# Kernel optimization log

Measured on AMD Instinct MI355X. Metric: run time of the kernel, lower is better.

## Reference

```python
import jax, jax.numpy as jnp
import numpy as np

STRIDE = 1
PADDING = 1


def sign_ste(w):
    # forward: 2*(w>0)-1 ; backward: identity (straight-through estimator)
    s = 2.0 * (w > 0.0).astype(w.dtype) - 1.0
    return w + jax.lax.stop_gradient(s - w)


def setup_inputs() -> dict:
    key = jax.random.key(0)
    kx, kw = jax.random.split(key)
    x = jax.random.normal(kx, (32, 256, 56, 56), dtype=jnp.float32)
    # mirror torch.rand(shape) * 0.001
    weight = jax.random.uniform(kw, (256, 256, 3, 3), dtype=jnp.float32) * 0.001
    return {"x": x, "weight": weight}


def reference(x, weight):
    # per-output-channel scaling factor: mean |w| over (in, kh, kw), detached
    scaling = jnp.mean(jnp.abs(weight), axis=(1, 2, 3), keepdims=True)  # [O,1,1,1]
    scaling = jax.lax.stop_gradient(scaling)
    binary_weights = scaling * sign_ste(weight)
    y = jax.lax.conv_general_dilated(
        x, binary_weights,
        window_strides=(STRIDE, STRIDE),
        padding=[(PADDING, PADDING), (PADDING, PADDING)],
        dimension_numbers=("NCHW", "OIHW", "NCHW"),
    )
    return y
```

## Files before the change

kernel.cpp:

```cpp
#include <hip/hip_runtime.h>
#include <stdint.h>


typedef float f32x4 __attribute__((ext_vector_type(4)));

__global__ __launch_bounds__(256) void stage1(const float* __restrict__ x,
                                              f32x4* __restrict__ u16,
                                              const float* __restrict__ w,
                                              float* __restrict__ scale,
                                              int* __restrict__ nneg,
                                              int* __restrict__ negidx) {
    __shared__ float red[4];
    __shared__ int cnt;
    if (blockIdx.x < 1568) {
        const int id  = blockIdx.x * 256 + threadIdx.x;
        const int n   = id / 12544;
        const int rem = id - n * 12544;
        const int g   = rem / 784;
        const int hw4 = rem - g * 784;
        const f32x4* xp =
            (const f32x4*)(x + (size_t)(n * 256 + g * 16) * 3136) + hw4;
        f32x4 s = {0.f, 0.f, 0.f, 0.f};
#pragma unroll
        for (int c = 0; c < 16; ++c)
            s += __builtin_nontemporal_load(xp + c * 784);
        u16[id] = s;
    } else {
        const int o = blockIdx.x - 1568, i = threadIdx.x;
        if (i == 0) cnt = 0;
        __syncthreads();
        const float* wp = w + ((size_t)o * 256 + i) * 9;
        float s = 0.f;
#pragma unroll
        for (int k = 0; k < 9; ++k) {
            const float v = wp[k];
            s += fabsf(v);
            if (v <= 0.f) {
                const int slot = atomicAdd(&cnt, 1);
                negidx[o * 2304 + slot] = i * 9 + k;
            }
        }
#pragma unroll
        for (int off = 32; off > 0; off >>= 1) s += __shfl_down(s, off);
        if ((i & 63) == 0) red[i >> 6] = s;
        __syncthreads();
        if (i == 0) {
            scale[o] = (red[0] + red[1] + red[2] + red[3]) * (1.0f / 2304.0f);
            nneg[o]  = cnt;
        }
    }
}

__global__ __launch_bounds__(256) void boxsum(const float* __restrict__ u16,
                                              float* __restrict__ T) {
    __shared__ float Us[336];
    const int n  = blockIdx.x / 14;
    const int h0 = (blockIdx.x - n * 14) * 4;
    const float* base = u16 + (size_t)n * 16 * 3136;
    for (int idx = threadIdx.x; idx < 336; idx += 256) {
        const int lr = idx / 56, col = idx - lr * 56;
        const int h = h0 - 1 + lr;
        float s = 0.f;
        if (h >= 0 && h < 56) {
            const float* bp = base + h * 56 + col;
#pragma unroll
            for (int g = 0; g < 16; ++g) s += bp[g * 3136];
        }
        Us[idx] = s;
    }
    __syncthreads();
    float* Tn = T + (size_t)n * 3136;
    for (int idx = threadIdx.x; idx < 224; idx += 256) {
        const int lr = idx / 56, w = idx - lr * 56;
        float acc = 0.f;
#pragma unroll
        for (int r = 0; r < 3; ++r) {
            const float* row = Us + (lr + r) * 56;
            if (w > 0)  acc += row[w - 1];
            acc += row[w];
            if (w < 55) acc += row[w + 1];
        }
        Tn[(h0 + lr) * 56 + w] = acc;
    }
}

__global__ __launch_bounds__(256) void yout(const float* __restrict__ T,
                                            const float* __restrict__ scale,
                                            const int* __restrict__ nneg,
                                            const int* __restrict__ negidx,
                                            const float* __restrict__ x,
                                            float* __restrict__ out) {
    const int b = blockIdx.x;
    const int o = b & 255, n = b >> 8;
    const float sc = scale[o];
    const f32x4* Tn = (const f32x4*)(T + (size_t)n * 3136);
    f32x4* op = (f32x4*)(out + ((size_t)n * 256 + o) * 3136);
    if (nneg[o] == 0) {
#pragma unroll
        for (int j = 0; j < 4; ++j) {
            const int hw4 = threadIdx.x + j * 256;
            if (hw4 >= 784) break;
            f32x4 v = Tn[hw4] * sc;
            __builtin_nontemporal_store(v, op + hw4);
        }
    } else {
        const int nn = nneg[o];
        const float c2 = 2.f * sc;
#pragma unroll
        for (int j = 0; j < 4; ++j) {
            const int hw4 = threadIdx.x + j * 256;
            if (hw4 >= 784) break;
            f32x4 v = Tn[hw4] * sc;
            for (int q = 0; q < nn; ++q) {
                const int iof = negidx[o * 2304 + q];
                const int i = iof / 9, rs = iof - i * 9;
                const int r = rs / 3 - 1, s2 = rs - (rs / 3) * 3 - 1;
                const float* xpl = x + ((size_t)n * 256 + i) * 3136;
#pragma unroll
                for (int e = 0; e < 4; ++e) {
                    const int hw = hw4 * 4 + e;
                    const int h = hw / 56 + r, ww = hw - (hw / 56) * 56 + s2;
                    const float xv = (h >= 0 && h < 56 && ww >= 0 && ww < 56)
                                         ? xpl[h * 56 + ww] : 0.f;
                    v[e] -= c2 * xv;
                }
            }
            __builtin_nontemporal_store(v, op + hw4);
        }
    }
}

extern "C" void kernel_launch(void* const* d_in, const int* in_sizes, int n_in,
                              void* d_out, int out_size, void* d_ws, size_t ws_size,
                              hipStream_t stream) {
    const float* x = (const float*)d_in[0];
    const float* w = (const float*)d_in[1];
    float* out = (float*)d_out;

    char* ws = (char*)d_ws;
    size_t off = 0;
    float* u16 = (float*)(ws + off);
    off += (size_t)32 * 16 * 3136 * 4;
    float* T = (float*)(ws + off);
    off += (size_t)32 * 3136 * 4;
    float* scale = (float*)(ws + off);
    off += 256 * 4;
    int* nneg = (int*)(ws + off);
    off += 256 * 4;
    int* negidx = (int*)(ws + off);

    stage1<<<dim3(1824), 256, 0, stream>>>(x, (f32x4*)u16, w, scale, nneg, negidx);
    boxsum<<<dim3(448), 256, 0, stream>>>(u16, T);
    yout<<<dim3(8192), 256, 0, stream>>>(T, scale, nneg, negidx, x, out);
}
```

Baseline: 178.3 us.

## Fuse box-sum and output-broadcast kernels into one per-row-tile kernel

Merges the boxsum and yout kernels into a single kernel. Each of the 448 blocks computes a 4-row tile of the 3x3 box sum into shared memory, then loops over all 256 output channels, writing scale*T plus any negative-weight corrections. This removes the global T buffer round trip and one kernel launch. In exchange the writes become scalar per-thread stores issued from far fewer blocks, each running a 256-iteration serial loop, which may reduce memory-level parallelism for the large output write.

```diff
diff --git a/kernel.cpp b/kernel.cpp
--- a/kernel.cpp
+++ b/kernel.cpp
@@ -51,13 +51,25 @@
     }
 }
 
-__global__ __launch_bounds__(256) void boxsum(const float* __restrict__ u16,
-                                              float* __restrict__ T) {
+__global__ __launch_bounds__(256) void boxout(const float* __restrict__ u16,
+                                              const float* __restrict__ scale,
+                                              const int* __restrict__ nneg,
+                                              const int* __restrict__ negidx,
+                                              const float* __restrict__ x,
+                                              float* __restrict__ out) {
     __shared__ float Us[336];
+    __shared__ float Tls[224];
+    __shared__ float ssc[256];
+    __shared__ int   snn[256];
     const int n  = blockIdx.x / 14;
     const int h0 = (blockIdx.x - n * 14) * 4;
+    const int t  = threadIdx.x;
+
+    ssc[t] = scale[t];
+    snn[t] = nneg[t];
+
     const float* base = u16 + (size_t)n * 16 * 3136;
-    for (int idx = threadIdx.x; idx < 336; idx += 256) {
+    for (int idx = t; idx < 336; idx += 256) {
         const int lr = idx / 56, col = idx - lr * 56;
         const int h = h0 - 1 + lr;
         float s = 0.f;
@@ -69,9 +81,8 @@
         Us[idx] = s;
     }
     __syncthreads();
-    float* Tn = T + (size_t)n * 3136;
-    for (int idx = threadIdx.x; idx < 224; idx += 256) {
-        const int lr = idx / 56, w = idx - lr * 56;
+    if (t < 224) {
+        const int lr = t / 56, w = t - lr * 56;
         float acc = 0.f;
 #pragma unroll
         for (int r = 0; r < 3; ++r) {
@@ -80,53 +91,32 @@
             acc += row[w];
             if (w < 55) acc += row[w + 1];
         }
-        Tn[(h0 + lr) * 56 + w] = acc;
+        Tls[t] = acc;
     }
-}
+    __syncthreads();
 
-__global__ __launch_bounds__(256) void yout(const float* __restrict__ T,
-                                            const float* __restrict__ scale,
-                                            const int* __restrict__ nneg,
-                                            const int* __restrict__ negidx,
-                                            const float* __restrict__ x,
-                                            float* __restrict__ out) {
-    const int b = blockIdx.x;
-    const int o = b & 255, n = b >> 8;
-    const float sc = scale[o];
-    const f32x4* Tn = (const f32x4*)(T + (size_t)n * 3136);
-    f32x4* op = (f32x4*)(out + ((size_t)n * 256 + o) * 3136);
-    if (nneg[o] == 0) {
-#pragma unroll
-        for (int j = 0; j < 4; ++j) {
-            const int hw4 = threadIdx.x + j * 256;
-            if (hw4 >= 784) break;
-            f32x4 v = Tn[hw4] * sc;
-            __builtin_nontemporal_store(v, op + hw4);
-        }
-    } else {
-        const int nn = nneg[o];
-        const float c2 = 2.f * sc;
-#pragma unroll
-        for (int j = 0; j < 4; ++j) {
-            const int hw4 = threadIdx.x + j * 256;
-            if (hw4 >= 784) break;
-            f32x4 v = Tn[hw4] * sc;
+    const float tv = (t < 224) ? Tls[t] : 0.f;
+    const int lr = t / 56, w = t - lr * 56, h = h0 + lr;
+    float* obase = out + (size_t)n * 256 * 3136 + h0 * 56;
+    for (int o = 0; o < 256; ++o) {
+        const float sc = ssc[o];
+        float v = sc * tv;
+        const int nn = snn[o];
+        if (nn > 0) {
+            const float c2 = 2.f * sc;
             for (int q = 0; q < nn; ++q) {
                 const int iof = negidx[o * 2304 + q];
                 const int i = iof / 9, rs = iof - i * 9;
                 const int r = rs / 3 - 1, s2 = rs - (rs / 3) * 3 - 1;
-                const float* xpl = x + ((size_t)n * 256 + i) * 3136;
-#pragma unroll
-                for (int e = 0; e < 4; ++e) {
-                    const int hw = hw4 * 4 + e;
-                    const int h = hw / 56 + r, ww = hw - (hw / 56) * 56 + s2;
-                    const float xv = (h >= 0 && h < 56 && ww >= 0 && ww < 56)
-                                         ? xpl[h * 56 + ww] : 0.f;
-                    v[e] -= c2 * xv;
-                }
+                const int hh = h + r, ww = w + s2;
+                const float xv = (hh >= 0 && hh < 56 && ww >= 0 && ww < 56)
+                                     ? x[((size_t)n * 256 + i) * 3136 + hh * 56 + ww]
+                                     : 0.f;
+                v -= c2 * xv;
             }
-            __builtin_nontemporal_store(v, op + hw4);
         }
+        if (t < 224)
+            __builtin_nontemporal_store(v, obase + (size_t)o * 3136 + t);
     }
 }
 
@@ -141,8 +131,6 @@
     size_t off = 0;
     float* u16 = (float*)(ws + off);
     off += (size_t)32 * 16 * 3136 * 4;
-    float* T = (float*)(ws + off);
-    off += (size_t)32 * 3136 * 4;
     float* scale = (float*)(ws + off);
     off += 256 * 4;
     int* nneg = (int*)(ws + off);
@@ -150,6 +138,5 @@
     int* negidx = (int*)(ws + off);
 
     stage1<<<dim3(1824), 256, 0, stream>>>(x, (f32x4*)u16, w, scale, nneg, negidx);
-    boxsum<<<dim3(448), 256, 0, stream>>>(u16, T);
-    yout<<<dim3(8192), 256, 0, stream>>>(T, scale, nneg, negidx, x, out);
+    boxout<<<dim3(448), 256, 0, stream>>>(u16, scale, nneg, negidx, x, out);
 }
```

Result: slower. 184.3 us (+3.4%).
